# Kernel optimization log

Measured on AMD Instinct MI355X. Metric: run time of the kernel, lower is better.

The kernel has to match this reference:

```python
import jax, jax.numpy as jnp
import numpy as np

EPS_FEAT = 1.0 + 1e-4   # feature_map offset: elu(x) + 1.0 + 0.0001
EPS_DEN = 1e-6


def setup_inputs() -> dict:
    key = jax.random.key(0)
    k1, k2, k3 = jax.random.split(key, 3)
    B, L, D = 4, 4096, 1024
    x = jax.random.normal(k1, (B, L, D), dtype=jnp.float32)
    # torch Linear-style init scale ~ 1/sqrt(fan_in)
    W_qkv = jax.random.normal(k2, (D, 3 * D), dtype=jnp.float32) / np.sqrt(D)
    b_qkv = jnp.zeros((3 * D,), dtype=jnp.float32)
    W_out = jax.random.normal(k3, (D, D), dtype=jnp.float32) / np.sqrt(D)
    b_out = jnp.zeros((D,), dtype=jnp.float32)
    return {"x": x, "W_qkv": W_qkv, "b_qkv": b_qkv, "W_out": W_out, "b_out": b_out}


def _linear_attention(x, W_qkv, b_qkv, W_out, b_out, num_heads=16):
    B, L, D = x.shape
    H = num_heads
    E = D // H

    qkv = x @ W_qkv + b_qkv                       # (B, L, 3D)
    q, k, v = jnp.split(qkv, 3, axis=-1)
    q = q.reshape(B, L, H, E)
    k = k.reshape(B, L, H, E)
    v = v.reshape(B, L, H, E)

    q = jax.nn.elu(q * (E ** -0.5)) + EPS_FEAT    # scale BEFORE feature map (as in source)
    k = jax.nn.elu(k) + EPS_FEAT

    # Causal linear attention via recurrence over L; math identical to
    # cumsum of k \otimes v outer products, but never materializes (B,L,H,E,E).
    qL = jnp.moveaxis(q, 1, 0)                    # (L, B, H, E)
    kL = jnp.moveaxis(k, 1, 0)
    vL = jnp.moveaxis(v, 1, 0)

    kv0 = jnp.zeros((B, H, E, E), dtype=x.dtype)
    ks0 = jnp.zeros((B, H, E), dtype=x.dtype)

    def step(carry, qkv_t):
        kv_s, k_s = carry
        q_t, k_t, v_t = qkv_t                     # each (B, H, E)
        kv_s = kv_s + jnp.einsum('bhe,bhf->bhef', k_t, v_t)
        k_s = k_s + k_t
        num = jnp.einsum('bhe,bhef->bhf', q_t, kv_s)           # (B, H, E)
        den = jnp.einsum('bhe,bhe->bh', q_t, k_s)[..., None] + EPS_DEN
        return (kv_s, k_s), num / den

    _, out = jax.lax.scan(step, (kv0, ks0), (qL, kL, vL))       # out: (L, B, H, E)
    out = jnp.moveaxis(out, 0, 1).reshape(B, L, D)
    # dropout is identity in eval mode
    return out @ W_out + b_out


def reference(x, W_qkv, b_qkv, W_out, b_out):
    return _linear_attention(x, W_qkv, b_qkv, W_out, b_out)
```

## Files before the change

kernel.cpp:

```cpp
#include <hip/hip_runtime.h>
#include <hip/hip_bf16.h>
#include <stdint.h>

#define B_ 4
#define L_ 4096
#define D_ 1024
#define H_ 16
#define E_ 64
#define M_ (B_*L_)
#define N1_ (3*D_)
#define CHK 128
#define NC (L_/CHK)
#define BH (B_*H_)

#define EPS_FEAT 1.0001f
#define EPS_DEN 1e-6f

typedef __attribute__((ext_vector_type(4))) float f32x4;
typedef __attribute__((ext_vector_type(8))) short bf16x8;

__device__ __forceinline__ unsigned short f2bf(float x) {
    union { float f; unsigned int u; } v; v.f = x;
    unsigned int r = v.u + 0x7FFFu + ((v.u >> 16) & 1u);
    return (unsigned short)(r >> 16);
}

__device__ __forceinline__ void gload_lds16(const unsigned short* g, unsigned short* l) {
    __builtin_amdgcn_global_load_lds(
        (const __attribute__((address_space(1))) unsigned int*)(const void*)g,
        (__attribute__((address_space(3))) unsigned int*)(void*)l,
        16, 0, 0);
}


__global__ __launch_bounds__(256) void prep(const float* __restrict__ x,
                                            const float* __restrict__ W0,
                                            const float* __restrict__ W1,
                                            unsigned short* __restrict__ xb,
                                            unsigned short* __restrict__ T0,
                                            unsigned short* __restrict__ T1) {
    __shared__ float tile[32][33];
    int bid = blockIdx.x, t = threadIdx.x;
    if (bid < 16384) {
        int i4 = bid * 256 + t;
        float4 v = ((const float4*)x)[i4];
        unsigned int lo = (unsigned int)f2bf(v.x) | ((unsigned int)f2bf(v.y) << 16);
        unsigned int hi = (unsigned int)f2bf(v.z) | ((unsigned int)f2bf(v.w) << 16);
        ((uint2*)xb)[i4] = make_uint2(lo, hi);
        return;
    }
    const float* W; unsigned short* WT; int N, nb, kb;
    if (bid < 16384 + 3072) {
        int idx = bid - 16384;
        W = W0; WT = T0; N = N1_;
        nb = (idx % 96) * 32; kb = (idx / 96) * 32;
    } else {
        int idx = bid - 16384 - 3072;
        W = W1; WT = T1; N = D_;
        nb = (idx % 32) * 32; kb = (idx / 32) * 32;
    }
    int tx = t & 31, ty = t >> 5;
#pragma unroll
    for (int j = 0; j < 4; ++j)
        tile[ty + 8*j][tx] = W[(size_t)(kb + ty + 8*j) * N + nb + tx];
    __syncthreads();
#pragma unroll
    for (int j = 0; j < 4; ++j) {
        int nl = ty + 8*j;
        WT[(size_t)(nb + nl) * D_ + kb + tx] = f2bf(tile[tx][nl]);
    }
}


template<int MODE, int KDIM, int NDIM>
__global__ __launch_bounds__(512, 2) void gemm256(
    const unsigned short* __restrict__ A,
    const unsigned short* __restrict__ BT,
    const float* __restrict__ bias,
    float* __restrict__ outF,
    unsigned short* __restrict__ qf,
    unsigned short* __restrict__ kf,
    unsigned short* __restrict__ vf)
{
    __shared__ __align__(16) unsigned short smem[65536];

    const int t = threadIdx.x, lane = t & 63, w = t >> 6;
    const int wr = w >> 2, wc = w & 3;

    const int nwgx = NDIM / 256;
    const int nwg = nwgx * (M_ / 256);
    const int bid0 = blockIdx.y * nwgx + blockIdx.x;
    const int swz = (bid0 & 7) * (nwg >> 3) + (bid0 >> 3);
    const int m0 = (swz / nwgx) * 256, n0 = (swz % nwgx) * 256;
    const int lr = lane & 15, lg = lane >> 4;

    auto stage = [&](int T, int ab, int h) {
        unsigned short* base = smem + (T & 1) * 32768 + ab * 16384 + h * 8192;
        const unsigned short* src = ab ? BT : A;
        const int boff = (ab ? n0 : m0) + h * 128;
        const int kt = T * 64;
#pragma unroll
        for (int i = 0; i < 2; ++i) {
            int c = i * 512 + t;
            int rowl = c >> 3, s = c & 7;
            int col = ((s ^ (rowl & 7)) << 3);
            gload_lds16(src + (size_t)(boff + rowl) * KDIM + kt + col, &base[c * 8]);
        }
    };

    f32x4 acc[8][4] = {};

    auto rdA = [&](const unsigned short* Ab, int m, int ks) {
        int row = wr * 128 + m * 16 + lr;
        int slot = (ks * 4 + lg) ^ (row & 7);
        return *(const bf16x8*)&Ab[row * 64 + slot * 8];
    };
    auto rdB = [&](const unsigned short* Bb, int n, int ks) {
        int row = wc * 64 + n * 16 + lr;
        int slot = (ks * 4 + lg) ^ (row & 7);
        return *(const bf16x8*)&Bb[row * 64 + slot * 8];
    };

    auto tile = [&](int T, bool s1, bool s2) {
        const unsigned short* Ab = smem + (T & 1) * 32768;
        const unsigned short* Bb = Ab + 16384;
        bf16x8 a0[4][2], bq[4][2];
#pragma unroll
        for (int m = 0; m < 4; ++m) { a0[m][0] = rdA(Ab, m, 0); a0[m][1] = rdA(Ab, m, 1); }
#pragma unroll
        for (int n = 0; n < 4; ++n) { bq[n][0] = rdB(Bb, n, 0); bq[n][1] = rdB(Bb, n, 1); }
        if (s1) { stage(T + 1, 0, 0); stage(T + 1, 0, 1); }
        __builtin_amdgcn_s_barrier();
        asm volatile("s_waitcnt lgkmcnt(0)" ::: "memory");
        __builtin_amdgcn_sched_barrier(0);
        __builtin_amdgcn_s_setprio(1);
        if (s2) { stage(T + 2, 1, 0); stage(T + 2, 1, 1); }
#pragma unroll
        for (int m = 0; m < 4; ++m)
#pragma unroll
            for (int n = 0; n < 4; ++n) {
                acc[m][n] = __builtin_amdgcn_mfma_f32_16x16x32_bf16(a0[m][0], bq[n][0], acc[m][n], 0, 0, 0);
                acc[m][n] = __builtin_amdgcn_mfma_f32_16x16x32_bf16(a0[m][1], bq[n][1], acc[m][n], 0, 0, 0);
            }
        bf16x8 a1[4][2];
#pragma unroll
        for (int m = 0; m < 4; ++m) { a1[m][0] = rdA(Ab, 4+m, 0); a1[m][1] = rdA(Ab, 4+m, 1); }
#pragma unroll
        for (int m = 0; m < 4; ++m)
#pragma unroll
            for (int n = 0; n < 4; ++n) {
                acc[4+m][n] = __builtin_amdgcn_mfma_f32_16x16x32_bf16(a1[m][0], bq[n][0], acc[4+m][n], 0, 0, 0);
                acc[4+m][n] = __builtin_amdgcn_mfma_f32_16x16x32_bf16(a1[m][1], bq[n][1], acc[4+m][n], 0, 0, 0);
            }
        __builtin_amdgcn_s_setprio(0);
    };

    constexpr int NT = KDIM / 64;
    stage(0, 0, 0); stage(0, 0, 1); stage(0, 1, 0); stage(0, 1, 1);
    stage(1, 1, 0); stage(1, 1, 1);
    asm volatile("s_waitcnt vmcnt(4)" ::: "memory");
    __builtin_amdgcn_s_barrier();
    __builtin_amdgcn_sched_barrier(0);

    for (int T = 0; T < NT - 2; ++T) {
        tile(T, true, true);
        asm volatile("s_waitcnt vmcnt(4)" ::: "memory");
        __builtin_amdgcn_s_barrier();
        __builtin_amdgcn_sched_barrier(0);
    }
    tile(NT - 2, true, false);
    asm volatile("s_waitcnt vmcnt(0)" ::: "memory");
    __builtin_amdgcn_s_barrier();
    __builtin_amdgcn_sched_barrier(0);
    tile(NT - 1, false, false);
    __syncthreads();

    if (MODE == 0) {
        unsigned short* cbf = smem;
        const bool isQ = (n0 < D_), isK = (n0 >= D_ && n0 < 2*D_);
        const float scale = isQ ? 0.125f : 1.0f;
        unsigned short* buf = isQ ? qf : (isK ? kf : vf);
        const int b = m0 >> 12, l0 = m0 & 4095;
        const int h0 = (n0 & 1023) >> 6;
#pragma unroll
        for (int p = 0; p < 2; ++p) {
            if (wr == p) {
#pragma unroll
                for (int n = 0; n < 4; ++n) {
                    int cl = wc*64 + n*16 + lr;
                    float bv = bias[n0 + cl];
#pragma unroll
                    for (int m = 0; m < 8; ++m)
#pragma unroll
                        for (int q = 0; q < 4; ++q) {
                            int rl = m*16 + lg*4 + q;
                            float val = (acc[m][n][q] + bv) * scale;
                            float fv = (isQ || isK)
                                       ? ((val > 0.f ? val : __expf(val) - 1.f) + EPS_FEAT)
                                       : val;
                            cbf[rl * 264 + cl] = f2bf(fv);
                        }
                }
            }
            __syncthreads();
#pragma unroll
            for (int hh = 0; hh < 4; ++hh) {
                unsigned short* dst = buf + (((size_t)(b * H_ + h0 + hh)) * L_ + l0 + p*128) * E_;
#pragma unroll
                for (int i = 0; i < 2; ++i) {
                    int c = i*512 + t, row = c >> 3, ch = c & 7;
                    uint4 v = *(const uint4*)&cbf[row * 264 + hh*64 + ch*8];
                    *(uint4*)&dst[row * 64 + ch*8] = v;
                }
            }
            __syncthreads();
        }
    } else {
        float* cfl = (float*)smem;
#pragma unroll
        for (int p = 0; p < 4; ++p) {
            if (wr == (p >> 1)) {
                int mbase = (p & 1) * 4;
#pragma unroll
                for (int n = 0; n < 4; ++n) {
                    int cl = wc*64 + n*16 + lr;
                    float bv = bias[n0 + cl];
#pragma unroll
                    for (int mm = 0; mm < 4; ++mm)
#pragma unroll
                        for (int q = 0; q < 4; ++q) {
                            int rl = mm*16 + lg*4 + q;
                            cfl[rl * 260 + cl] = acc[mbase + mm][n][q] + bv;
                        }
                }
            }
            __syncthreads();
#pragma unroll
            for (int i = 0; i < 8; ++i) {
                int c = i*512 + t, row = c >> 6, ch = c & 63;
                float4 v = *(const float4*)&cfl[row * 260 + ch*4];
                *(float4*)&outF[(size_t)(m0 + p*64 + row) * NDIM + n0 + ch*4] = v;
            }
            __syncthreads();
        }
    }
}


__global__ __launch_bounds__(256) void chunk_kv(
    const unsigned short* __restrict__ kf, const unsigned short* __restrict__ vf,
    unsigned short* __restrict__ kvout, float* __restrict__ ksout)
{
    constexpr int LDK = 136;
    __shared__ unsigned short Kt[64 * LDK];
    __shared__ unsigned short Vt[80 * LDK];

    int t = threadIdx.x, lane = t & 63, w = t >> 6;
    int bid = blockIdx.x;
    const unsigned short* kp = kf + (size_t)bid * CHK * E_;
    const unsigned short* vp = vf + (size_t)bid * CHK * E_;

#pragma unroll
    for (int it = 0; it < 4; ++it) {
        int s = it * 256 + t;
        int rl = s >> 3, e0 = (s & 7) << 3;
        uint4 kv8 = *(const uint4*)(kp + s * 8);
        uint4 vv8 = *(const uint4*)(vp + s * 8);
        unsigned int kw[4] = {kv8.x, kv8.y, kv8.z, kv8.w};
        unsigned int vw[4] = {vv8.x, vv8.y, vv8.z, vv8.w};
#pragma unroll
        for (int jw = 0; jw < 4; ++jw) {
            Kt[(e0 + 2*jw    ) * LDK + rl] = (unsigned short)(kw[jw] & 0xFFFF);
            Kt[(e0 + 2*jw + 1) * LDK + rl] = (unsigned short)(kw[jw] >> 16);
            Vt[(e0 + 2*jw    ) * LDK + rl] = (unsigned short)(vw[jw] & 0xFFFF);
            Vt[(e0 + 2*jw + 1) * LDK + rl] = (unsigned short)(vw[jw] >> 16);
        }
    }
    if (t < 128) Vt[64 * LDK + t] = 0x3F80;
    for (int i = t; i < 15 * LDK; i += 256) Vt[65 * LDK + i] = 0;
    __syncthreads();

    int lr = lane & 15, lg = lane >> 4;
    f32x4 acc[4] = {};
    f32x4 accE[4] = {};
#pragma unroll
    for (int ks = 0; ks < 4; ++ks) {
        bf16x8 a = *(const bf16x8*)&Vt[(w*16 + lr) * LDK + ks*32 + lg*8];
#pragma unroll
        for (int n = 0; n < 4; ++n) {
            bf16x8 b = *(const bf16x8*)&Kt[(n*16 + lr) * LDK + ks*32 + lg*8];
            acc[n] = __builtin_amdgcn_mfma_f32_16x16x32_bf16(a, b, acc[n], 0, 0, 0);
        }
    }
    if (w == 0) {
#pragma unroll
        for (int ks = 0; ks < 4; ++ks) {
            bf16x8 a = *(const bf16x8*)&Vt[(64 + lr) * LDK + ks*32 + lg*8];
#pragma unroll
            for (int n = 0; n < 4; ++n) {
                bf16x8 b = *(const bf16x8*)&Kt[(n*16 + lr) * LDK + ks*32 + lg*8];
                accE[n] = __builtin_amdgcn_mfma_f32_16x16x32_bf16(a, b, accE[n], 0, 0, 0);
            }
        }
    }
    unsigned short* kvo = kvout + (size_t)bid * E_ * E_;
#pragma unroll
    for (int n = 0; n < 4; ++n)
#pragma unroll
        for (int q = 0; q < 4; ++q) {
            int f = w*16 + lg*4 + q, e = n*16 + lr;
            kvo[f * 64 + e] = f2bf(acc[n][q]);
        }
    if (w == 0 && lg == 0) {
#pragma unroll
        for (int n = 0; n < 4; ++n)
            ksout[(size_t)bid * 64 + n*16 + lr] = accE[n][0];
    }
}


__global__ __launch_bounds__(256) void prefix_kv(
    const uint2* __restrict__ kvin, const float* __restrict__ ks,
    uint2* __restrict__ kvb, unsigned short* __restrict__ ksb)
{
    int bh = blockIdx.y, part = blockIdx.x, t = threadIdx.x;
    int idx = part * 256 + t;
    float st0 = 0.f, st1 = 0.f, st2 = 0.f, st3 = 0.f;
    for (int c = 0; c < NC; ++c) {
        size_t o = ((size_t)bh * NC + c) * 1024 + idx;
        uint2 tmp = kvin[o];
        kvb[o] = make_uint2(
            (unsigned int)f2bf(st0) | ((unsigned int)f2bf(st1) << 16),
            (unsigned int)f2bf(st2) | ((unsigned int)f2bf(st3) << 16));
        union { unsigned int u; float f; } cv;
        cv.u = (tmp.x & 0xFFFFu) << 16; st0 += cv.f;
        cv.u = tmp.x & 0xFFFF0000u;     st1 += cv.f;
        cv.u = (tmp.y & 0xFFFFu) << 16; st2 += cv.f;
        cv.u = tmp.y & 0xFFFF0000u;     st3 += cv.f;
    }
    if (part == 0 && t < 64) {
        float s0 = 0.f;
        for (int c = 0; c < NC; ++c) {
            float tmp = ks[((size_t)bh * NC + c) * 64 + t];
            ksb[((size_t)bh * NC + c) * 64 + t] = f2bf(s0);
            s0 += tmp;
        }
    }
}


__global__ __launch_bounds__(256, 2) void attn_out(
    const unsigned short* __restrict__ qf, const unsigned short* __restrict__ kf,
    const unsigned short* __restrict__ vf, const unsigned short* __restrict__ kvb,
    const unsigned short* __restrict__ ksb, unsigned short* __restrict__ attn)
{
    constexpr int LK = 72;
    constexpr int LV = 136;
    __shared__ unsigned short Ks[128 * LK];
    __shared__ unsigned short Vt[64 * LV];
    __shared__ unsigned short Ss[128 * LV];

    int t = threadIdx.x, lane = t & 63, w = t >> 6;
    int bid = blockIdx.x;
    int bh = bid >> 5, c = bid & 31;
    const unsigned short* qp = qf + (size_t)bid * CHK * E_;
    const unsigned short* kp = kf + (size_t)bid * CHK * E_;
    const unsigned short* vp = vf + (size_t)bid * CHK * E_;
    const unsigned short* kvp = kvb + (size_t)bid * 4096;

    int lr = lane & 15, lg = lane >> 4;
    const int jsel[2] = {w, 7 - w};

    bf16x8 aq[2][2];
#pragma unroll
    for (int mi = 0; mi < 2; ++mi)
#pragma unroll
        for (int ks = 0; ks < 2; ++ks)
            aq[mi][ks] = *(const bf16x8*)(qp + (jsel[mi]*16 + lr) * 64 + ks*32 + lg*8);

#pragma unroll
    for (int it = 0; it < 4; ++it) {
        int s = it * 256 + t;
        int r = s >> 3, e0 = (s & 7) << 3;
        uint4 kv = *(const uint4*)(kp + s * 8);
        uint4 vv = *(const uint4*)(vp + s * 8);
        *(uint4*)&Ks[r * LK + e0] = kv;
        unsigned int vw[4] = {vv.x, vv.y, vv.z, vv.w};
#pragma unroll
        for (int jw = 0; jw < 4; ++jw) {
            Vt[(e0 + 2*jw    ) * LV + r] = (unsigned short)(vw[jw] & 0xFFFF);
            Vt[(e0 + 2*jw + 1) * LV + r] = (unsigned short)(vw[jw] >> 16);
        }
    }
    bf16x8 zfrag = {0,0,0,0,0,0,0,0};
    bf16x8 bone = zfrag, bks[2] = {zfrag, zfrag};
    if (lr == 0) {
#pragma unroll
        for (int j = 0; j < 8; ++j) bone[j] = (short)0x3F80;
        bks[0] = *(const bf16x8*)&ksb[(size_t)bid * 64 + lg*8];
        bks[1] = *(const bf16x8*)&ksb[(size_t)bid * 64 + 32 + lg*8];
    }
    __syncthreads();

#pragma unroll
    for (int mi = 0; mi < 2; ++mi) {
        int j = jsel[mi];
        int rbase = j * 16;
        int jbmax = j | 1;
        for (int jb = 0; jb <= jbmax; ++jb) {
            if (jb <= j) {
                f32x4 sacc = {};
                bf16x8 b0 = *(const bf16x8*)&Ks[(jb*16 + lr) * LK + lg*8];
                bf16x8 b1 = *(const bf16x8*)&Ks[(jb*16 + lr) * LK + 32 + lg*8];
                sacc = __builtin_amdgcn_mfma_f32_16x16x32_bf16(aq[mi][0], b0, sacc, 0, 0, 0);
                sacc = __builtin_amdgcn_mfma_f32_16x16x32_bf16(aq[mi][1], b1, sacc, 0, 0, 0);
#pragma unroll
                for (int q = 0; q < 4; ++q) {
                    int r = rbase + lg*4 + q;
                    int jj = jb*16 + lr;
                    Ss[r * LV + jj] = (jj <= r) ? f2bf(sacc[q]) : (unsigned short)0;
                }
            } else {
#pragma unroll
                for (int q = 0; q < 4; ++q) {
                    int r = rbase + lg*4 + q;
                    Ss[r * LV + jb*16 + lr] = 0;
                }
            }
        }
    }

    f32x4 oacc[2][5] = {};
#pragma unroll
    for (int mi = 0; mi < 2; ++mi) {
        int j = jsel[mi];
        int rbase = j * 16;
#pragma unroll
        for (int ks = 0; ks < 2; ++ks) {
            bf16x8 a = aq[mi][ks];
#pragma unroll
            for (int n = 0; n < 4; ++n) {
                bf16x8 b = *(const bf16x8*)&kvp[(n*16 + lr) * 64 + ks*32 + lg*8];
                oacc[mi][n] = __builtin_amdgcn_mfma_f32_16x16x32_bf16(a, b, oacc[mi][n], 0, 0, 0);
            }
            oacc[mi][4] = __builtin_amdgcn_mfma_f32_16x16x32_bf16(a, bks[ks], oacc[mi][4], 0, 0, 0);
        }
        for (int ks = 0; ks <= (j >> 1); ++ks) {
            bf16x8 a = *(const bf16x8*)&Ss[(rbase + lr) * LV + ks*32 + lg*8];
#pragma unroll
            for (int n = 0; n < 4; ++n) {
                bf16x8 b = *(const bf16x8*)&Vt[(n*16 + lr) * LV + ks*32 + lg*8];
                oacc[mi][n] = __builtin_amdgcn_mfma_f32_16x16x32_bf16(a, b, oacc[mi][n], 0, 0, 0);
            }
            oacc[mi][4] = __builtin_amdgcn_mfma_f32_16x16x32_bf16(a, bone, oacc[mi][4], 0, 0, 0);
        }
    }

    int b_idx = bh >> 4, h_idx = bh & 15;
#pragma unroll
    for (int mi = 0; mi < 2; ++mi) {
        int rbase = jsel[mi] * 16;
        float den[4];
#pragma unroll
        for (int q = 0; q < 4; ++q)
            den[q] = __shfl(oacc[mi][4][q], lane & 48, 64) + EPS_DEN;
#pragma unroll
        for (int n = 0; n < 4; ++n) {
#pragma unroll
            for (int q = 0; q < 4; ++q) {
                int r = rbase + lg*4 + q;
                int lpos = c * CHK + r;
                int col = n*16 + lr;
                size_t dst = ((size_t)b_idx * L_ + lpos) * D_ + h_idx * 64 + col;
                attn[dst] = f2bf(oacc[mi][n][q] / den[q]);
            }
        }
    }
}


extern "C" void kernel_launch(void* const* d_in, const int* in_sizes, int n_in,
                              void* d_out, int out_size, void* d_ws, size_t ws_size,
                              hipStream_t stream)
{
    const float* x    = (const float*)d_in[0];
    const float* Wqkv = (const float*)d_in[1];
    const float* bqkv = (const float*)d_in[2];
    const float* Wout = (const float*)d_in[3];
    const float* bout = (const float*)d_in[4];
    float* out = (float*)d_out;

    char* ws = (char*)d_ws;
    size_t off = 0;
    auto alloc = [&](size_t bytes) { void* p = ws + off; off += (bytes + 255) & ~(size_t)255; return p; };
    unsigned short* xb  = (unsigned short*)alloc((size_t)M_ * D_ * 2);
    unsigned short* WqT = (unsigned short*)alloc((size_t)N1_ * D_ * 2);
    unsigned short* WoT = (unsigned short*)alloc((size_t)D_ * D_ * 2);
    unsigned short* qfb = (unsigned short*)alloc((size_t)M_ * D_ * 2);
    unsigned short* kfb = (unsigned short*)alloc((size_t)M_ * D_ * 2);
    unsigned short* vfb = (unsigned short*)alloc((size_t)M_ * D_ * 2);
    unsigned short* kvw = (unsigned short*)alloc((size_t)BH * NC * E_ * E_ * 2);
    float* ksw = (float*)alloc((size_t)BH * NC * E_ * 4);
    unsigned short* kvb = (unsigned short*)alloc((size_t)BH * NC * E_ * E_ * 2);
    unsigned short* ksb = (unsigned short*)alloc((size_t)BH * NC * E_ * 2);
    unsigned short* attn = xb;

    prep<<<16384 + 3072 + 1024, 256, 0, stream>>>(x, Wqkv, Wout, xb, WqT, WoT);

    gemm256<0, D_, N1_><<<dim3(N1_ / 256, M_ / 256), 512, 0, stream>>>(
        xb, WqT, bqkv, nullptr, qfb, kfb, vfb);

    chunk_kv<<<BH * NC, 256, 0, stream>>>(kfb, vfb, kvw, ksw);
    prefix_kv<<<dim3(4, BH), 256, 0, stream>>>((const uint2*)kvw, ksw, (uint2*)kvb, ksb);
    attn_out<<<BH * NC, 256, 0, stream>>>(qfb, kfb, vfb, kvb, ksb, attn);

    gemm256<1, D_, D_><<<dim3(D_ / 256, M_ / 256), 512, 0, stream>>>(
        attn, WoT, bout, out, nullptr, nullptr, nullptr);
}
```

Measured before the change: 240.4 us.

## Replace 256x256 GEMM tile with 128x256 tile and triple-buffered K=32 pipeline

The projection GEMMs move from 512-thread 256x256 tiles with a two-stage K=64 double buffer to 256-thread 128x256 tiles with a three-stage K=32 ring buffer. Each wave now owns a 128x64 output slab, and the epilogues are reworked to match. The smaller LDS footprint and doubled grid aim to raise occupancy and wave-level parallelism. In exchange there is less data reuse per tile, more barrier round-trips per unit of K, and more global traffic for the operand re-reads.

```diff
diff --git a/kernel.cpp b/kernel.cpp
--- a/kernel.cpp
+++ b/kernel.cpp
@@ -73,7 +73,7 @@
 
 
 template<int MODE, int KDIM, int NDIM>
-__global__ __launch_bounds__(512, 2) void gemm256(
+__global__ __launch_bounds__(256, 2) void gemm128(
     const unsigned short* __restrict__ A,
     const unsigned short* __restrict__ BT,
     const float* __restrict__ bias,
@@ -82,97 +82,85 @@
     unsigned short* __restrict__ kf,
     unsigned short* __restrict__ vf)
 {
-    __shared__ __align__(16) unsigned short smem[65536];
+    __shared__ __align__(16) unsigned short smem[36864];
 
     const int t = threadIdx.x, lane = t & 63, w = t >> 6;
-    const int wr = w >> 2, wc = w & 3;
 
     const int nwgx = NDIM / 256;
-    const int nwg = nwgx * (M_ / 256);
+    const int nwg = nwgx * (M_ / 128);
     const int bid0 = blockIdx.y * nwgx + blockIdx.x;
     const int swz = (bid0 & 7) * (nwg >> 3) + (bid0 >> 3);
-    const int m0 = (swz / nwgx) * 256, n0 = (swz % nwgx) * 256;
+    const int m0 = (swz / nwgx) * 128, n0 = (swz % nwgx) * 256;
     const int lr = lane & 15, lg = lane >> 4;
 
-    auto stage = [&](int T, int ab, int h) {
-        unsigned short* base = smem + (T & 1) * 32768 + ab * 16384 + h * 8192;
-        const unsigned short* src = ab ? BT : A;
-        const int boff = (ab ? n0 : m0) + h * 128;
-        const int kt = T * 64;
+    auto stage = [&](int T) {
+        unsigned short* base = smem + (T % 3) * 12288;
+        const int kt = T * 32;
 #pragma unroll
         for (int i = 0; i < 2; ++i) {
-            int c = i * 512 + t;
-            int rowl = c >> 3, s = c & 7;
-            int col = ((s ^ (rowl & 7)) << 3);
-            gload_lds16(src + (size_t)(boff + rowl) * KDIM + kt + col, &base[c * 8]);
+            int c = i * 256 + t;
+            int row = c >> 2, s = c & 3;
+            int col = ((s ^ ((row >> 1) & 3)) << 3);
+            gload_lds16(A + (size_t)(m0 + row) * KDIM + kt + col, &base[c * 8]);
+        }
+        unsigned short* bb = base + 4096;
+#pragma unroll
+        for (int i = 0; i < 4; ++i) {
+            int c = i * 256 + t;
+            int row = c >> 2, s = c & 3;
+            int col = ((s ^ ((row >> 1) & 3)) << 3);
+            gload_lds16(BT + (size_t)(n0 + row) * KDIM + kt + col, &bb[c * 8]);
         }
     };
 
     f32x4 acc[8][4] = {};
 
-    auto rdA = [&](const unsigned short* Ab, int m, int ks) {
-        int row = wr * 128 + m * 16 + lr;
-        int slot = (ks * 4 + lg) ^ (row & 7);
-        return *(const bf16x8*)&Ab[row * 64 + slot * 8];
-    };
-    auto rdB = [&](const unsigned short* Bb, int n, int ks) {
-        int row = wc * 64 + n * 16 + lr;
-        int slot = (ks * 4 + lg) ^ (row & 7);
-        return *(const bf16x8*)&Bb[row * 64 + slot * 8];
-    };
-
-    auto tile = [&](int T, bool s1, bool s2) {
-        const unsigned short* Ab = smem + (T & 1) * 32768;
-        const unsigned short* Bb = Ab + 16384;
-        bf16x8 a0[4][2], bq[4][2];
-#pragma unroll
-        for (int m = 0; m < 4; ++m) { a0[m][0] = rdA(Ab, m, 0); a0[m][1] = rdA(Ab, m, 1); }
-#pragma unroll
-        for (int n = 0; n < 4; ++n) { bq[n][0] = rdB(Bb, n, 0); bq[n][1] = rdB(Bb, n, 1); }
-        if (s1) { stage(T + 1, 0, 0); stage(T + 1, 0, 1); }
+    auto tile = [&](int T, bool s1) {
+        const unsigned short* Ab = smem + (T % 3) * 12288;
+        const unsigned short* Bb = Ab + 4096;
+        bf16x8 af[8], bq[4];
+#pragma unroll
+        for (int m = 0; m < 8; ++m) {
+            int row = m * 16 + lr;
+            int slot = lg ^ ((row >> 1) & 3);
+            af[m] = *(const bf16x8*)&Ab[row * 32 + slot * 8];
+        }
+#pragma unroll
+        for (int n = 0; n < 4; ++n) {
+            int row = w * 64 + n * 16 + lr;
+            int slot = lg ^ ((row >> 1) & 3);
+            bq[n] = *(const bf16x8*)&Bb[row * 32 + slot * 8];
+        }
+        if (s1) stage(T + 2);
         __builtin_amdgcn_s_barrier();
         asm volatile("s_waitcnt lgkmcnt(0)" ::: "memory");
         __builtin_amdgcn_sched_barrier(0);
         __builtin_amdgcn_s_setprio(1);
-        if (s2) { stage(T + 2, 1, 0); stage(T + 2, 1, 1); }
-#pragma unroll
-        for (int m = 0; m < 4; ++m)
-#pragma unroll
-            for (int n = 0; n < 4; ++n) {
-                acc[m][n] = __builtin_amdgcn_mfma_f32_16x16x32_bf16(a0[m][0], bq[n][0], acc[m][n], 0, 0, 0);
-                acc[m][n] = __builtin_amdgcn_mfma_f32_16x16x32_bf16(a0[m][1], bq[n][1], acc[m][n], 0, 0, 0);
-            }
-        bf16x8 a1[4][2];
-#pragma unroll
-        for (int m = 0; m < 4; ++m) { a1[m][0] = rdA(Ab, 4+m, 0); a1[m][1] = rdA(Ab, 4+m, 1); }
-#pragma unroll
-        for (int m = 0; m < 4; ++m)
-#pragma unroll
-            for (int n = 0; n < 4; ++n) {
-                acc[4+m][n] = __builtin_amdgcn_mfma_f32_16x16x32_bf16(a1[m][0], bq[n][0], acc[4+m][n], 0, 0, 0);
-                acc[4+m][n] = __builtin_amdgcn_mfma_f32_16x16x32_bf16(a1[m][1], bq[n][1], acc[4+m][n], 0, 0, 0);
-            }
+#pragma unroll
+        for (int m = 0; m < 8; ++m)
+#pragma unroll
+            for (int n = 0; n < 4; ++n)
+                acc[m][n] = __builtin_amdgcn_mfma_f32_16x16x32_bf16(af[m], bq[n], acc[m][n], 0, 0, 0);
         __builtin_amdgcn_s_setprio(0);
     };
 
-    constexpr int NT = KDIM / 64;
-    stage(0, 0, 0); stage(0, 0, 1); stage(0, 1, 0); stage(0, 1, 1);
-    stage(1, 1, 0); stage(1, 1, 1);
-    asm volatile("s_waitcnt vmcnt(4)" ::: "memory");
+    constexpr int NT = KDIM / 32;
+    stage(0); stage(1);
+    asm volatile("s_waitcnt vmcnt(6)" ::: "memory");
     __builtin_amdgcn_s_barrier();
     __builtin_amdgcn_sched_barrier(0);
 
     for (int T = 0; T < NT - 2; ++T) {
-        tile(T, true, true);
-        asm volatile("s_waitcnt vmcnt(4)" ::: "memory");
+        tile(T, true);
+        asm volatile("s_waitcnt vmcnt(6)" ::: "memory");
         __builtin_amdgcn_s_barrier();
         __builtin_amdgcn_sched_barrier(0);
     }
-    tile(NT - 2, true, false);
+    tile(NT - 2, false);
     asm volatile("s_waitcnt vmcnt(0)" ::: "memory");
     __builtin_amdgcn_s_barrier();
     __builtin_amdgcn_sched_barrier(0);
-    tile(NT - 1, false, false);
+    tile(NT - 1, false);
     __syncthreads();
 
     if (MODE == 0) {
@@ -183,61 +171,52 @@
         const int b = m0 >> 12, l0 = m0 & 4095;
         const int h0 = (n0 & 1023) >> 6;
 #pragma unroll
-        for (int p = 0; p < 2; ++p) {
-            if (wr == p) {
-#pragma unroll
-                for (int n = 0; n < 4; ++n) {
-                    int cl = wc*64 + n*16 + lr;
-                    float bv = bias[n0 + cl];
-#pragma unroll
-                    for (int m = 0; m < 8; ++m)
-#pragma unroll
-                        for (int q = 0; q < 4; ++q) {
-                            int rl = m*16 + lg*4 + q;
-                            float val = (acc[m][n][q] + bv) * scale;
-                            float fv = (isQ || isK)
-                                       ? ((val > 0.f ? val : __expf(val) - 1.f) + EPS_FEAT)
-                                       : val;
-                            cbf[rl * 264 + cl] = f2bf(fv);
-                        }
+        for (int n = 0; n < 4; ++n) {
+            int cl = w*64 + n*16 + lr;
+            float bv = bias[n0 + cl];
+#pragma unroll
+            for (int m = 0; m < 8; ++m)
+#pragma unroll
+                for (int q = 0; q < 4; ++q) {
+                    int rl = m*16 + lg*4 + q;
+                    float val = (acc[m][n][q] + bv) * scale;
+                    float fv = (isQ || isK)
+                               ? ((val > 0.f ? val : __expf(val) - 1.f) + EPS_FEAT)
+                               : val;
+                    cbf[rl * 264 + cl] = f2bf(fv);
                 }
-            }
-            __syncthreads();
-#pragma unroll
-            for (int hh = 0; hh < 4; ++hh) {
-                unsigned short* dst = buf + (((size_t)(b * H_ + h0 + hh)) * L_ + l0 + p*128) * E_;
-#pragma unroll
-                for (int i = 0; i < 2; ++i) {
-                    int c = i*512 + t, row = c >> 3, ch = c & 7;
-                    uint4 v = *(const uint4*)&cbf[row * 264 + hh*64 + ch*8];
-                    *(uint4*)&dst[row * 64 + ch*8] = v;
-                }
-            }
-            __syncthreads();
+        }
+        __syncthreads();
+#pragma unroll
+        for (int hh = 0; hh < 4; ++hh) {
+            unsigned short* dst = buf + (((size_t)(b * H_ + h0 + hh)) * L_ + l0) * E_;
+#pragma unroll
+            for (int i = 0; i < 4; ++i) {
+                int c = i*256 + t, row = c >> 3, ch = c & 7;
+                uint4 v = *(const uint4*)&cbf[row * 264 + hh*64 + ch*8];
+                *(uint4*)&dst[row * 64 + ch*8] = v;
+            }
         }
     } else {
         float* cfl = (float*)smem;
 #pragma unroll
-        for (int p = 0; p < 4; ++p) {
-            if (wr == (p >> 1)) {
-                int mbase = (p & 1) * 4;
-#pragma unroll
-                for (int n = 0; n < 4; ++n) {
-                    int cl = wc*64 + n*16 + lr;
-                    float bv = bias[n0 + cl];
-#pragma unroll
-                    for (int mm = 0; mm < 4; ++mm)
-#pragma unroll
-                        for (int q = 0; q < 4; ++q) {
-                            int rl = mm*16 + lg*4 + q;
-                            cfl[rl * 260 + cl] = acc[mbase + mm][n][q] + bv;
-                        }
-                }
+        for (int p = 0; p < 2; ++p) {
+#pragma unroll
+            for (int n = 0; n < 4; ++n) {
+                int cl = w*64 + n*16 + lr;
+                float bv = bias[n0 + cl];
+#pragma unroll
+                for (int mm = 0; mm < 4; ++mm)
+#pragma unroll
+                    for (int q = 0; q < 4; ++q) {
+                        int rl = mm*16 + lg*4 + q;
+                        cfl[rl * 260 + cl] = acc[p*4 + mm][n][q] + bv;
+                    }
             }
             __syncthreads();
 #pragma unroll
-            for (int i = 0; i < 8; ++i) {
-                int c = i*512 + t, row = c >> 6, ch = c & 63;
+            for (int i = 0; i < 16; ++i) {
+                int c = i*256 + t, row = c >> 6, ch = c & 63;
                 float4 v = *(const float4*)&cfl[row * 260 + ch*4];
                 *(float4*)&outF[(size_t)(m0 + p*64 + row) * NDIM + n0 + ch*4] = v;
             }
@@ -507,13 +486,13 @@
 
     prep<<<16384 + 3072 + 1024, 256, 0, stream>>>(x, Wqkv, Wout, xb, WqT, WoT);
 
-    gemm256<0, D_, N1_><<<dim3(N1_ / 256, M_ / 256), 512, 0, stream>>>(
+    gemm128<0, D_, N1_><<<dim3(N1_ / 256, M_ / 128), 256, 0, stream>>>(
         xb, WqT, bqkv, nullptr, qfb, kfb, vfb);
 
     chunk_kv<<<BH * NC, 256, 0, stream>>>(kfb, vfb, kvw, ksw);
     prefix_kv<<<dim3(4, BH), 256, 0, stream>>>((const uint2*)kvw, ksw, (uint2*)kvb, ksb);
     attn_out<<<BH * NC, 256, 0, stream>>>(qfb, kfb, vfb, kvb, ksb, attn);
 
-    gemm256<1, D_, D_><<<dim3(D_ / 256, M_ / 256), 512, 0, stream>>>(
+    gemm128<1, D_, D_><<<dim3(D_ / 256, M_ / 128), 256, 0, stream>>>(
         attn, WoT, bout, out, nullptr, nullptr, nullptr);
 }
```

Result: faster. 235.3 us (median of 2 runs) (-2.1%).
